# Kernel tuning notes

Hardware: AMD Instinct MI355X
Metric: run time of the kernel (lower is better)

## Reference

```python
import jax, jax.numpy as jnp
import numpy as np

IN_FEATURES = 8192
OUT_FEATURES = 28672
RANK = 32
GROUP = 64          # int4 quantization group size along in_features
M_TOKENS = 16       # decode-style batch of tokens
PAD = 128           # kernel requires in dim padded to multiple of 128


def setup_inputs() -> dict:
    key = jax.random.key(0)
    k0, k1, k2, k3, k4, k5 = jax.random.split(key, 6)
    x = jax.random.normal(k0, (M_TOKENS, IN_FEATURES), dtype=jnp.float16)
    # int4 codes in [-8, 7], stored unpacked as int32
    qweight = jax.random.randint(k1, (OUT_FEATURES, IN_FEATURES), 0, 16, dtype=jnp.int32) - 8
    # positive per-(out_channel, group) dequant scales, realistic small magnitude
    wscales = (jax.random.uniform(k2, (OUT_FEATURES, IN_FEATURES // GROUP), dtype=jnp.float16)
               * jnp.float16(0.02) + jnp.float16(0.001))
    # low-rank SVD correction branch (LoRA-style)
    lora_down = jax.random.normal(k3, (RANK, IN_FEATURES), dtype=jnp.float16) * jnp.float16(0.02)
    lora_up = jax.random.normal(k4, (OUT_FEATURES, RANK), dtype=jnp.float16) * jnp.float16(0.02)
    bias = jax.random.normal(k5, (OUT_FEATURES,), dtype=jnp.float16)
    return {"x": x, "qweight": qweight, "wscales": wscales,
            "lora_down": lora_down, "lora_up": lora_up, "bias": bias}


def reference(x, qweight, wscales, lora_down, lora_up, bias):
    # Pad input features to a multiple of 128 (as the CUDA kernel requires).
    in_pad = ((IN_FEATURES + PAD - 1) // PAD) * PAD
    if x.shape[-1] != in_pad:
        x = jnp.pad(x, ((0, 0), (0, in_pad - x.shape[-1])))
    xk = x[:, :IN_FEATURES]  # padded columns hit zero weight columns; equivalent

    # Dequantize: W[o, k] = q[o, k] * scale[o, k // GROUP]   -> [out, in] fp16
    w = qweight.astype(jnp.float16) * jnp.repeat(wscales, GROUP, axis=1)

    # Quantized GEMM + low-rank correction + bias (all fused in the real kernel)
    y = jnp.matmul(xk, w.T)                                   # [M, out]
    y = y + jnp.matmul(jnp.matmul(xk, lora_down.T), lora_up.T)  # rank-RANK branch
    y = y + bias
    return y[:, :OUT_FEATURES]
```

## Files before the change

kernel.cpp:

```cpp
#include <hip/hip_runtime.h>
#include <hip/hip_bf16.h>

#define IN_F 8192
#define OUT_F 28672
#define RANK 32
#define NGROUPS 128
#define M_TOK 16
#define TCHUNK 16
#define TCK (IN_F / TCHUNK)
#define KSPLIT 4
#define KW (IN_F / KSPLIT)
#define NSTEP (KW / 256)

typedef __bf16 bf16x8 __attribute__((ext_vector_type(8)));
typedef float  f32x4  __attribute__((ext_vector_type(4)));
typedef int    i32x4  __attribute__((ext_vector_type(4)));

#define GLOBAL_AS __attribute__((address_space(1)))
#define LDS_AS    __attribute__((address_space(3)))

__global__ __launch_bounds__(512) void svdq_prep(
    const float* __restrict__ x, const float* __restrict__ ld,
    float* __restrict__ part, __bf16* __restrict__ xb) {
  const int c = blockIdx.x;
  const int i = threadIdx.x;

  {
    const int base = c * 8192 + i * 16;
    f32x4 f0 = *reinterpret_cast<const f32x4*>(x + base);
    f32x4 f1 = *reinterpret_cast<const f32x4*>(x + base + 4);
    f32x4 f2 = *reinterpret_cast<const f32x4*>(x + base + 8);
    f32x4 f3 = *reinterpret_cast<const f32x4*>(x + base + 12);
    bf16x8 v0, v1;
#pragma unroll
    for (int j = 0; j < 4; ++j) {
      v0[j] = (__bf16)f0[j]; v0[j + 4] = (__bf16)f1[j];
      v1[j] = (__bf16)f2[j]; v1[j + 4] = (__bf16)f3[j];
    }
    *reinterpret_cast<bf16x8*>(xb + base)     = v0;
    *reinterpret_cast<bf16x8*>(xb + base + 8) = v1;
  }

  const int m = i >> 5, r = i & 31;
  const f32x4* xp = reinterpret_cast<const f32x4*>(x  + (size_t)m * IN_F + c * TCK);
  const f32x4* lp = reinterpret_cast<const f32x4*>(ld + (size_t)r * IN_F + c * TCK);
  float s = 0.f;
#pragma unroll 8
  for (int j = 0; j < TCK / 4; ++j) {
    f32x4 a = xp[j], b = lp[j];
    s += a[0]*b[0] + a[1]*b[1] + a[2]*b[2] + a[3]*b[3];
  }
  part[(size_t)c * (M_TOK * RANK) + i] = s;
}

__global__ __launch_bounds__(256) void svdq_main(
    const __bf16* __restrict__ xb, const int* __restrict__ qw,
    const float* __restrict__ wsc, const float* __restrict__ lu,
    const float* __restrict__ bias, const float* __restrict__ part,
    float* __restrict__ out) {
  const int w     = threadIdx.x >> 6;
  const int lane  = threadIdx.x & 63;
  const int col   = lane & 15;
  const int hi    = lane >> 4;
  const int obase = blockIdx.x * 16;
  const int o     = obase + col;

  __shared__ int smem[KSPLIT * 8192];
  int* mybuf = smem + w * 8192;

  const int*    qbase = qw + (size_t)obase * IN_F + w * KW;
  const __bf16* xrow  = xb + (size_t)col * IN_F + w * KW + hi * 8;
  const float*  srow  = wsc + (size_t)o * NGROUPS + w * (KW / 64);

  int xoff[8];
#pragma unroll
  for (int j = 0; j < 8; ++j) xoff[j] = (lane ^ j) * 4;

#define STAGE(T, B)                                                            \
  {                                                                            \
    _Pragma("unroll")                                                          \
    for (int r = 0; r < 16; ++r) {                                             \
      const int* _s = qbase + (size_t)r * IN_F + (T) * 256 + xoff[r & 7];      \
      __builtin_amdgcn_global_load_lds((const GLOBAL_AS int*)_s,               \
          (LDS_AS int*)(mybuf + (B) * 4096 + r * 256), 16, 0, 0);              \
    }                                                                          \
  }

  f32x4 acc = {0.f, 0.f, 0.f, 0.f};

#define COMPUTE(B, AX, SC)                                                     \
  {                                                                            \
    const int* _base = mybuf + (B) * 4096 + col * 256;                         \
    const int  _sw   = col & 7;                                                \
    _Pragma("unroll")                                                          \
    for (int kk = 0; kk < 8; ++kk) {                                           \
      const int c0 = kk * 8 + hi * 2;                                          \
      i32x4 q0 = *reinterpret_cast<const i32x4*>(_base + ((c0 ^ _sw) * 4));    \
      i32x4 q1 = *reinterpret_cast<const i32x4*>(_base + (((c0 + 1) ^ _sw) * 4));\
      const float s = (SC)[kk >> 1];                                           \
      bf16x8 b;                                                                \
      _Pragma("unroll")                                                        \
      for (int j = 0; j < 4; ++j) {                                            \
        b[j]     = (__bf16)((float)q0[j] * s);                                 \
        b[j + 4] = (__bf16)((float)q1[j] * s);                                 \
      }                                                                        \
      acc = __builtin_amdgcn_mfma_f32_16x16x32_bf16((AX)[kk], b, acc, 0, 0, 0);\
    }                                                                          \
  }

#define LOADX(AX, T)                                                           \
  {                                                                            \
    _Pragma("unroll")                                                          \
    for (int kk = 0; kk < 8; ++kk)                                             \
      (AX)[kk] = *reinterpret_cast<const bf16x8*>(xrow + (T) * 256 + kk * 32); \
  }

  STAGE(0, 0)
  bf16x8 acur[8], anext[8];
  LOADX(acur, 0)
  f32x4 sc = *reinterpret_cast<const f32x4*>(srow);

#pragma unroll 1
  for (int t = 0; t < NSTEP - 1; ++t) {
    LOADX(anext, t + 1)
    f32x4 sn = *reinterpret_cast<const f32x4*>(srow + (t + 1) * 4);
    STAGE(t + 1, (t + 1) & 1)
    asm volatile("s_waitcnt vmcnt(25)" ::: "memory");
    __builtin_amdgcn_sched_barrier(0);
    COMPUTE(t & 1, acur, sc)
#pragma unroll
    for (int kk = 0; kk < 8; ++kk) acur[kk] = anext[kk];
    sc = sn;
  }
  asm volatile("s_waitcnt vmcnt(0)" ::: "memory");
  __builtin_amdgcn_sched_barrier(0);
  COMPUTE((NSTEP - 1) & 1, acur, sc)

#undef STAGE
#undef COMPUTE
#undef LOADX

  __syncthreads();
  float* red = reinterpret_cast<float*>(smem);
#pragma unroll
  for (int r = 0; r < 4; ++r) red[(w * 64 + lane) * 4 + r] = acc[r];
  __syncthreads();
  if (threadIdx.x >= 64) return;

  f32x4 tot = {0.f, 0.f, 0.f, 0.f};
#pragma unroll
  for (int ww = 0; ww < KSPLIT; ++ww)
    tot += *reinterpret_cast<const f32x4*>(red + (ww * 64 + lane) * 4);

  f32x4 t0 = {0.f,0.f,0.f,0.f}, t1 = {0.f,0.f,0.f,0.f};
#pragma unroll
  for (int c = 0; c < TCHUNK; ++c) {
    const f32x4* pc = reinterpret_cast<const f32x4*>(
        part + (size_t)c * (M_TOK * RANK) + col * RANK + hi * 8);
    t0 += pc[0];
    t1 += pc[1];
  }
  f32x4 u0 = *reinterpret_cast<const f32x4*>(lu + (size_t)o * RANK + hi * 8);
  f32x4 u1 = *reinterpret_cast<const f32x4*>(lu + (size_t)o * RANK + hi * 8 + 4);
  bf16x8 ta, lb;
#pragma unroll
  for (int j = 0; j < 4; ++j) {
    ta[j]     = (__bf16)t0[j];
    ta[j + 4] = (__bf16)t1[j];
    lb[j]     = (__bf16)u0[j];
    lb[j + 4] = (__bf16)u1[j];
  }
  f32x4 lacc = {0.f, 0.f, 0.f, 0.f};
  lacc = __builtin_amdgcn_mfma_f32_16x16x32_bf16(ta, lb, lacc, 0, 0, 0);

  const float bv = bias[o];
#pragma unroll
  for (int reg = 0; reg < 4; ++reg) {
    const int m = hi * 4 + reg;
    out[(size_t)m * OUT_F + o] = tot[reg] + lacc[reg] + bv;
  }
}

extern "C" void kernel_launch(void* const* d_in, const int* in_sizes, int n_in,
                              void* d_out, int out_size, void* d_ws, size_t ws_size,
                              hipStream_t stream) {
  const float* x    = (const float*)d_in[0];
  const int*   qw   = (const int*)d_in[1];
  const float* wsc  = (const float*)d_in[2];
  const float* ld   = (const float*)d_in[3];
  const float* lu   = (const float*)d_in[4];
  const float* bias = (const float*)d_in[5];
  float*       out  = (float*)d_out;

  float*  part = (float*)d_ws;
  __bf16* xbf  = (__bf16*)((char*)d_ws + 64 * 1024);

  svdq_prep<<<TCHUNK, 512, 0, stream>>>(x, ld, part, xbf);
  svdq_main<<<OUT_F / 16, 256, 0, stream>>>(xbf, qw, wsc, lu, bias, part, out);
}
```

Measured before the change: 221.7 us.

## Share a 3-stage LDS ring across waves instead of per-wave K-split buffers

Previously each of 4 waves owned a private double-buffered 32KB slice per K-split. Now the four waves cooperatively stage each 256-wide K tile of all 16 rows into a shared triple-buffered ring (48KB total), and each wave computes its own 64-wide sub-slice of every tile. Cross-wave barriers plus vmcnt waits manage the ring. The smaller LDS footprint (128KB down to 48KB) should allow more resident blocks and so more memory-level parallelism, at the cost of a block-wide barrier every step.

```diff
diff --git a/kernel.cpp b/kernel.cpp
--- a/kernel.cpp
+++ b/kernel.cpp
@@ -8,9 +8,8 @@
 #define M_TOK 16
 #define TCHUNK 16
 #define TCK (IN_F / TCHUNK)
-#define KSPLIT 4
-#define KW (IN_F / KSPLIT)
-#define NSTEP (KW / 256)
+#define NS 32
+#define SS 256
 
 typedef __bf16 bf16x8 __attribute__((ext_vector_type(8)));
 typedef float  f32x4  __attribute__((ext_vector_type(4)));
@@ -65,80 +64,92 @@
   const int obase = blockIdx.x * 16;
   const int o     = obase + col;
 
-  __shared__ int smem[KSPLIT * 8192];
-  int* mybuf = smem + w * 8192;
-
-  const int*    qbase = qw + (size_t)obase * IN_F + w * KW;
-  const __bf16* xrow  = xb + (size_t)col * IN_F + w * KW + hi * 8;
-  const float*  srow  = wsc + (size_t)o * NGROUPS + w * (KW / 64);
-
-  int xoff[8];
-#pragma unroll
-  for (int j = 0; j < 8; ++j) xoff[j] = (lane ^ j) * 4;
+  __shared__ int smem[3 * 4096];
+
+  const int*    qb   = qw + (size_t)obase * IN_F;
+  const __bf16* xrow = xb + (size_t)col * IN_F + hi * 8;
+  const float*  srow = wsc + (size_t)o * NGROUPS;
 
 #define STAGE(T, B)                                                            \
   {                                                                            \
     _Pragma("unroll")                                                          \
-    for (int r = 0; r < 16; ++r) {                                             \
-      const int* _s = qbase + (size_t)r * IN_F + (T) * 256 + xoff[r & 7];      \
+    for (int j = 0; j < 4; ++j) {                                              \
+      const int r = w * 4 + j;                                                 \
+      const int* _s = qb + (size_t)r * IN_F + (T) * SS + ((lane ^ (r & 7)) << 2);\
       __builtin_amdgcn_global_load_lds((const GLOBAL_AS int*)_s,               \
-          (LDS_AS int*)(mybuf + (B) * 4096 + r * 256), 16, 0, 0);              \
+          (LDS_AS int*)(smem + (B) * 4096 + r * 256), 16, 0, 0);               \
     }                                                                          \
   }
 
+#define XLOAD(T, A0, A1, S)                                                    \
+  {                                                                            \
+    (A0) = *reinterpret_cast<const bf16x8*>(xrow + (T) * SS + w * 64);         \
+    (A1) = *reinterpret_cast<const bf16x8*>(xrow + (T) * SS + w * 64 + 32);    \
+    (S)  = srow[(T) * 4 + w];                                                  \
+  }
+
   f32x4 acc = {0.f, 0.f, 0.f, 0.f};
 
-#define COMPUTE(B, AX, SC)                                                     \
+#define COMPUTE(CB, A0, A1, S)                                                 \
   {                                                                            \
-    const int* _base = mybuf + (B) * 4096 + col * 256;                         \
+    const int* _base = smem + (CB) * 4096 + col * 256;                         \
     const int  _sw   = col & 7;                                                \
     _Pragma("unroll")                                                          \
-    for (int kk = 0; kk < 8; ++kk) {                                           \
-      const int c0 = kk * 8 + hi * 2;                                          \
-      i32x4 q0 = *reinterpret_cast<const i32x4*>(_base + ((c0 ^ _sw) * 4));    \
-      i32x4 q1 = *reinterpret_cast<const i32x4*>(_base + (((c0 + 1) ^ _sw) * 4));\
-      const float s = (SC)[kk >> 1];                                           \
+    for (int kk = 0; kk < 2; ++kk) {                                           \
+      const int c0 = w * 16 + kk * 8 + hi * 2;                                 \
+      i32x4 q0 = *reinterpret_cast<const i32x4*>(_base + ((c0 ^ _sw) << 2));   \
+      i32x4 q1 = *reinterpret_cast<const i32x4*>(_base + (((c0 + 1) ^ _sw) << 2));\
       bf16x8 b;                                                                \
       _Pragma("unroll")                                                        \
-      for (int j = 0; j < 4; ++j) {                                            \
-        b[j]     = (__bf16)((float)q0[j] * s);                                 \
-        b[j + 4] = (__bf16)((float)q1[j] * s);                                 \
+      for (int jj = 0; jj < 4; ++jj) {                                         \
+        b[jj]     = (__bf16)((float)q0[jj] * (S));                             \
+        b[jj + 4] = (__bf16)((float)q1[jj] * (S));                             \
       }                                                                        \
-      acc = __builtin_amdgcn_mfma_f32_16x16x32_bf16((AX)[kk], b, acc, 0, 0, 0);\
+      acc = __builtin_amdgcn_mfma_f32_16x16x32_bf16(kk ? (A1) : (A0), b, acc,  \
+                                                    0, 0, 0);                  \
     }                                                                          \
   }
 
-#define LOADX(AX, T)                                                           \
-  {                                                                            \
-    _Pragma("unroll")                                                          \
-    for (int kk = 0; kk < 8; ++kk)                                             \
-      (AX)[kk] = *reinterpret_cast<const bf16x8*>(xrow + (T) * 256 + kk * 32); \
-  }
+  bf16x8 a0, a1, a0n, a1n;
+  float  sc, scn;
 
   STAGE(0, 0)
-  bf16x8 acur[8], anext[8];
-  LOADX(acur, 0)
-  f32x4 sc = *reinterpret_cast<const f32x4*>(srow);
-
+  asm volatile("" ::: "memory");
+  XLOAD(0, a0, a1, sc)
+  asm volatile("" ::: "memory");
+  STAGE(1, 1)
+  asm volatile("s_waitcnt vmcnt(7)" ::: "memory");
+  __builtin_amdgcn_s_barrier();
+
+  int cb = 0, sb = 2;
 #pragma unroll 1
-  for (int t = 0; t < NSTEP - 1; ++t) {
-    LOADX(anext, t + 1)
-    f32x4 sn = *reinterpret_cast<const f32x4*>(srow + (t + 1) * 4);
-    STAGE(t + 1, (t + 1) & 1)
-    asm volatile("s_waitcnt vmcnt(25)" ::: "memory");
+  for (int t = 0; t + 2 < NS; ++t) {
+    XLOAD(t + 1, a0n, a1n, scn)
+    STAGE(t + 2, sb)
+    asm volatile("s_waitcnt vmcnt(14)" ::: "memory");
     __builtin_amdgcn_sched_barrier(0);
-    COMPUTE(t & 1, acur, sc)
-#pragma unroll
-    for (int kk = 0; kk < 8; ++kk) acur[kk] = anext[kk];
-    sc = sn;
-  }
+    COMPUTE(cb, a0, a1, sc)
+    asm volatile("s_waitcnt vmcnt(7)" ::: "memory");
+    __builtin_amdgcn_s_barrier();
+    a0 = a0n; a1 = a1n; sc = scn;
+    cb = (cb == 2) ? 0 : cb + 1;
+    sb = (sb == 2) ? 0 : sb + 1;
+  }
+  XLOAD(NS - 1, a0n, a1n, scn)
+  asm volatile("s_waitcnt vmcnt(10)" ::: "memory");
+  __builtin_amdgcn_sched_barrier(0);
+  COMPUTE(cb, a0, a1, sc)
+  asm volatile("s_waitcnt vmcnt(3)" ::: "memory");
+  __builtin_amdgcn_s_barrier();
+  a0 = a0n; a1 = a1n; sc = scn;
+  cb = (cb == 2) ? 0 : cb + 1;
   asm volatile("s_waitcnt vmcnt(0)" ::: "memory");
   __builtin_amdgcn_sched_barrier(0);
-  COMPUTE((NSTEP - 1) & 1, acur, sc)
+  COMPUTE(cb, a0, a1, sc)
 
 #undef STAGE
+#undef XLOAD
 #undef COMPUTE
-#undef LOADX
 
   __syncthreads();
   float* red = reinterpret_cast<float*>(smem);
@@ -149,7 +160,7 @@
 
   f32x4 tot = {0.f, 0.f, 0.f, 0.f};
 #pragma unroll
-  for (int ww = 0; ww < KSPLIT; ++ww)
+  for (int ww = 0; ww < 4; ++ww)
     tot += *reinterpret_cast<const f32x4*>(red + (ww * 64 + lane) * 4);
 
   f32x4 t0 = {0.f,0.f,0.f,0.f}, t1 = {0.f,0.f,0.f,0.f};
```

After: 238.2 us. +7.4%, slower.
